# Optimization experiments

Measured on AMD Instinct MI355X. Metric: run time of the kernel, lower is better.

The kernel has to match this reference:

```python
import jax, jax.numpy as jnp
import numpy as np

B, T, M, VM = 64, 512, 8, 50  # batch, time, num_modules, rois per module
EPS = 1e-5  # BatchNorm eps


def setup_inputs() -> dict:
    key = jax.random.key(0)
    ks = jax.random.split(key, 12)
    x = jax.random.normal(ks[0], (B, M * VM, T, 1), jnp.float32)
    # learned adjacency, torch init = ones/V; perturb slightly
    PA = jnp.full((M, VM, VM), 1.0 / VM, jnp.float32) + 0.01 * jax.random.normal(ks[1], (M, VM, VM), jnp.float32)
    conv_w = jax.random.normal(ks[2], (M,), jnp.float32)          # 1x1 conv weight (1->1 chan) per module
    conv_b = 0.1 * jax.random.normal(ks[3], (M,), jnp.float32)
    bn_gamma = 1.0 + 0.1 * jax.random.normal(ks[4], (M,), jnp.float32)
    bn_beta = 0.1 * jax.random.normal(ks[5], (M,), jnp.float32)
    bn_mean = 0.1 * jax.random.normal(ks[6], (M,), jnp.float32)
    bn_var = jax.random.uniform(ks[7], (M,), jnp.float32) + 0.5   # positive
    w1 = jax.random.normal(ks[8], (M, 8), jnp.float32) * 0.5      # Linear(1,8) weight per module
    b1 = 0.1 * jax.random.normal(ks[9], (M, 8), jnp.float32)
    w2 = jax.random.normal(ks[10], (M, 8), jnp.float32) * 0.5     # Linear(8,1) weight per module
    b2 = 0.1 * jax.random.normal(ks[11], (M,), jnp.float32)
    return dict(x=x, PA=PA, conv_w=conv_w, conv_b=conv_b, bn_gamma=bn_gamma, bn_beta=bn_beta,
                bn_mean=bn_mean, bn_var=bn_var, w1=w1, b1=b1, w2=w2, b2=b2)


def reference(x, PA, conv_w, conv_b, bn_gamma, bn_beta, bn_mean, bn_var, w1, b1, w2, b2):
    # x: [B, V_total, T, 1]; torch permute(0,3,2,1) -> [B, C=1, T, V_total]
    xp = x[..., 0].transpose(0, 2, 1)                 # [B, T, V_total]
    xm = xp.reshape(B, T, M, VM)                      # contiguous module blocks == index_select
    # UnitGCN: x_agg = x @ A per module
    agg = jnp.einsum('btmv,mvw->btmw', xm, PA)        # [B, T, M, VM]
    # 1x1 conv (scalar per module) + BatchNorm2d(1) in eval mode + ReLU
    y = agg * conv_w[:, None] + conv_b[:, None]
    scale = bn_gamma / jnp.sqrt(bn_var + EPS)
    h = jax.nn.relu((y - bn_mean[:, None]) * scale[:, None] + bn_beta[:, None])
    # AttentionPooling: MLP(1->8->1) on channel dim, softmax over nodes, weighted sum
    hid = jnp.tanh(h[..., None] * w1[:, None, :] + b1[:, None, :])   # [B, T, M, VM, 8]
    score = jnp.einsum('btmvh,mh->btmv', hid, w2) + b2[:, None]      # [B, T, M, VM]
    attn = jax.nn.softmax(score, axis=3)
    pooled = jnp.sum(h * attn, axis=3)                # [B, T, M]
    # concat over modules on dim 1 -> [B, M, T, 1]
    return pooled.transpose(0, 2, 1)[..., None]
```

## Files before the change

kernel.cpp:

```cpp
#include <hip/hip_runtime.h>

#define BB 64
#define TT 512
#define MM 8
#define VMM 50
#define KP 64
#define NP 64
#define RSTRIDE 36
#define EPSV 1e-5f

#define TN   1024
#define HMAX 16.0f
#define HSTEP (HMAX / TN)
#define INVH  (TN / HMAX)

using short8  = __attribute__((ext_vector_type(8))) short;
using float4v = __attribute__((ext_vector_type(4))) float;

__device__ __forceinline__ float fast_rcp(float x) {
    return __builtin_amdgcn_rcpf(x);
}
__device__ __forceinline__ float fast_tanh(float x) {
    float e2 = __expf(2.0f * x);
    return fmaf(-2.0f, fast_rcp(e2 + 1.0f), 1.0f);
}
__device__ __forceinline__ unsigned f2bf(float f) {
    unsigned u = __float_as_uint(f);
    return (u + 0x7FFFu + ((u >> 16) & 1u)) >> 16;
}
__device__ __forceinline__ unsigned pack2(float lo, float hi) {
    return f2bf(lo) | (f2bf(hi) << 16);
}

__global__ __launch_bounds__(256, 2)
void intra_module_agg_kernel(const float* __restrict__ x,
                             const float* __restrict__ PA,
                             const float* __restrict__ conv_w,
                             const float* __restrict__ conv_b,
                             const float* __restrict__ bn_gamma,
                             const float* __restrict__ bn_beta,
                             const float* __restrict__ bn_mean,
                             const float* __restrict__ bn_var,
                             const float* __restrict__ w1,
                             const float* __restrict__ b1,
                             const float* __restrict__ w2,
                             const float* __restrict__ b2,
                             float* __restrict__ out)
{
    const int blk = blockIdx.x;
    const int tt  = blk & 1;
    const int m   = (blk >> 1) & 7;
    const int b   = blk >> 4;
    const int j   = threadIdx.x;

    __shared__ __align__(16) unsigned xsu[256 * RSTRIDE];
    __shared__ __align__(16) unsigned psu[NP * RSTRIDE];
    __shared__ float  graw[TN + 1];
    __shared__ float2 gtab[TN];

    const float scale = bn_gamma[m] * __frsqrt_rn(bn_var[m] + EPSV);
    const float Amul  = conv_w[m] * scale;
    const float Cadd  = (conv_b[m] - bn_mean[m]) * scale + bn_beta[m];

    {
        const float* xb = x + ((b * (MM * VMM) + m * VMM) * TT + tt * 256 + j);
#pragma unroll
        for (int vp = 0; vp < 25; ++vp) {
            float a = xb[(2 * vp) * TT];
            float c = xb[(2 * vp + 1) * TT];
            xsu[j * RSTRIDE + vp] = pack2(a, c);
        }
#pragma unroll
        for (int vp = 25; vp < 32; ++vp) xsu[j * RSTRIDE + vp] = 0u;
    }

    {
        const float* pa = PA + m * (VMM * VMM);
        const int w  = j & 63;
        const int vb = (j >> 6) * 8;
#pragma unroll
        for (int i = 0; i < 8; ++i) {
            int vp = vb + i, v0 = 2 * vp, v1 = v0 + 1;
            float a = (w < VMM && v0 < VMM) ? pa[v0 * VMM + w] : 0.0f;
            float c = (w < VMM && v1 < VMM) ? pa[v1 * VMM + w] : 0.0f;
            psu[w * RSTRIDE + vp] = pack2(a, c);
        }
    }

    {
        const float B2 = b2[m];
        for (int i = j; i < TN + 1; i += 256) {
            float h = i * HSTEP;
            float s = B2;
#pragma unroll
            for (int k = 0; k < 8; ++k)
                s = fmaf(w2[m * 8 + k],
                         fast_tanh(fmaf(h, w1[m * 8 + k], b1[m * 8 + k])), s);
            graw[i] = __expf(s);
        }
    }
    __syncthreads();

    for (int i = j; i < TN; i += 256)
        gtab[i] = make_float2(graw[i], graw[i + 1] - graw[i]);

    const int lane = j & 63, wv = j >> 6;
    const int q = lane >> 4, nl = lane & 15;

    short8 Bf[4][2];
#pragma unroll
    for (int nt = 0; nt < 4; ++nt)
#pragma unroll
        for (int ks = 0; ks < 2; ++ks)
            Bf[nt][ks] = *(const short8*)&psu[(nt * 16 + nl) * RSTRIDE + ks * 16 + q * 4];

    float4v C[4][4];
#pragma unroll
    for (int mt = 0; mt < 4; ++mt)
#pragma unroll
        for (int nt = 0; nt < 4; ++nt)
            C[mt][nt] = (float4v){0.f, 0.f, 0.f, 0.f};

#pragma unroll
    for (int mt = 0; mt < 4; ++mt) {
        const int row = (wv * 4 + mt) * 16 + nl;
        short8 A0 = *(const short8*)&xsu[row * RSTRIDE + 0 * 16 + q * 4];
        short8 A1 = *(const short8*)&xsu[row * RSTRIDE + 1 * 16 + q * 4];
#pragma unroll
        for (int nt = 0; nt < 4; ++nt) {
            C[mt][nt] = __builtin_amdgcn_mfma_f32_16x16x32_bf16(A0, Bf[nt][0], C[mt][nt], 0, 0, 0);
            C[mt][nt] = __builtin_amdgcn_mfma_f32_16x16x32_bf16(A1, Bf[nt][1], C[mt][nt], 0, 0, 0);
        }
    }
    __syncthreads();

    const int obase = (b * MM + m) * TT + tt * 256;
#pragma unroll
    for (int mt = 0; mt < 4; ++mt) {
        float se[4] = {0.f, 0.f, 0.f, 0.f};
        float sh[4] = {0.f, 0.f, 0.f, 0.f};
#pragma unroll
        for (int nt = 0; nt < 4; ++nt) {
            const bool ok = (nt * 16 + nl) < VMM;
#pragma unroll
            for (int r = 0; r < 4; ++r) {
                float h = fmaxf(fmaf(C[mt][nt][r], Amul, Cadd), 0.0f);
                float u = fminf(h, HMAX - 0.0005f) * INVH;
                int   i = (int)u;
                float fr = u - (float)i;
                float2 p = gtab[i];
                float e = ok ? fmaf(fr, p.y, p.x) : 0.0f;
                se[r] += e;
                sh[r] = fmaf(h, e, sh[r]);
            }
        }
#pragma unroll
        for (int r = 0; r < 4; ++r) {
#pragma unroll
            for (int mk = 1; mk < 16; mk <<= 1) {
                se[r] += __shfl_xor(se[r], mk, 64);
                sh[r] += __shfl_xor(sh[r], mk, 64);
            }
        }
        if (nl == 0) {
#pragma unroll
            for (int r = 0; r < 4; ++r)
                out[obase + (wv * 4 + mt) * 16 + q * 4 + r] = sh[r] * fast_rcp(se[r]);
        }
    }
}

extern "C" void kernel_launch(void* const* d_in, const int* in_sizes, int n_in,
                              void* d_out, int out_size, void* d_ws, size_t ws_size,
                              hipStream_t stream) {
    const float* x        = (const float*)d_in[0];
    const float* PA       = (const float*)d_in[1];
    const float* conv_w   = (const float*)d_in[2];
    const float* conv_b   = (const float*)d_in[3];
    const float* bn_gamma = (const float*)d_in[4];
    const float* bn_beta  = (const float*)d_in[5];
    const float* bn_mean  = (const float*)d_in[6];
    const float* bn_var   = (const float*)d_in[7];
    const float* w1       = (const float*)d_in[8];
    const float* b1       = (const float*)d_in[9];
    const float* w2       = (const float*)d_in[10];
    const float* b2       = (const float*)d_in[11];
    float* out = (float*)d_out;

    dim3 grid(BB * MM * (TT / 256));
    dim3 block(256);
    intra_module_agg_kernel<<<grid, block, 0, stream>>>(
        x, PA, conv_w, conv_b, bn_gamma, bn_beta, bn_mean, bn_var,
        w1, b1, w2, b2, out);
}
```

Before: 116.3 us.

## Halve time tile, transpose MFMA roles, pack fp16 softmax table

Each block now covers 128 time steps instead of 256, so the grid doubles and launch bounds allow 4 blocks per CU. The MFMA operands are swapped so PA is the A operand and x is B. Each lane then holds one time step across many nodes, which cuts the softmax reduction from 4-step shuffles to 2. The exp-score lookup table is built in a single pass into fp16-packed pairs, with a shifted exponent for range, which drops one shared buffer and one barrier. The risks are fp16 precision loss in the table and possible bank conflicts in the new LDS access pattern.

```diff
diff --git a/kernel.cpp b/kernel.cpp
--- a/kernel.cpp
+++ b/kernel.cpp
@@ -4,8 +4,7 @@
 #define TT 512
 #define MM 8
 #define VMM 50
-#define KP 64
-#define NP 64
+#define TBLK 128
 #define RSTRIDE 36
 #define EPSV 1e-5f
 
@@ -31,8 +30,19 @@
 __device__ __forceinline__ unsigned pack2(float lo, float hi) {
     return f2bf(lo) | (f2bf(hi) << 16);
 }
-
-__global__ __launch_bounds__(256, 2)
+__device__ __forceinline__ unsigned packh2(float lo, float hi) {
+    unsigned short a = __builtin_bit_cast(unsigned short, (_Float16)lo);
+    unsigned short b = __builtin_bit_cast(unsigned short, (_Float16)hi);
+    return (unsigned)a | ((unsigned)b << 16);
+}
+__device__ __forceinline__ float h2f_lo(unsigned p) {
+    return (float)__builtin_bit_cast(_Float16, (unsigned short)(p & 0xFFFFu));
+}
+__device__ __forceinline__ float h2f_hi(unsigned p) {
+    return (float)__builtin_bit_cast(_Float16, (unsigned short)(p >> 16));
+}
+
+__global__ __launch_bounds__(256, 4)
 void intra_module_agg_kernel(const float* __restrict__ x,
                              const float* __restrict__ PA,
                              const float* __restrict__ conv_w,
@@ -48,30 +58,36 @@
                              float* __restrict__ out)
 {
     const int blk = blockIdx.x;
-    const int tt  = blk & 1;
-    const int m   = (blk >> 1) & 7;
-    const int b   = blk >> 4;
+    const int tq  = blk & 3;
+    const int m   = (blk >> 2) & 7;
+    const int b   = blk >> 5;
     const int j   = threadIdx.x;
 
-    __shared__ __align__(16) unsigned xsu[256 * RSTRIDE];
-    __shared__ __align__(16) unsigned psu[NP * RSTRIDE];
-    __shared__ float  graw[TN + 1];
-    __shared__ float2 gtab[TN];
+    __shared__ __align__(16) unsigned xsu[TBLK * RSTRIDE];
+    __shared__ __align__(16) unsigned psu[64 * RSTRIDE];
+    __shared__ unsigned gt[TN];
 
     const float scale = bn_gamma[m] * __frsqrt_rn(bn_var[m] + EPSV);
     const float Amul  = conv_w[m] * scale;
     const float Cadd  = (conv_b[m] - bn_mean[m]) * scale + bn_beta[m];
 
     {
-        const float* xb = x + ((b * (MM * VMM) + m * VMM) * TT + tt * 256 + j);
-#pragma unroll
-        for (int vp = 0; vp < 25; ++vp) {
-            float a = xb[(2 * vp) * TT];
-            float c = xb[(2 * vp + 1) * TT];
-            xsu[j * RSTRIDE + vp] = pack2(a, c);
-        }
-#pragma unroll
-        for (int vp = 25; vp < 32; ++vp) xsu[j * RSTRIDE + vp] = 0u;
+        const int t  = j >> 1;
+        const int hf = j & 1;
+        const float* xb = x + ((b * (MM * VMM) + m * VMM) * TT + tq * TBLK + t);
+        unsigned* row = &xsu[t * RSTRIDE];
+        const int vp0 = hf * 13;
+#pragma unroll
+        for (int i = 0; i < 13; ++i) {
+            int vp = vp0 + i;
+            float a = 0.0f, c = 0.0f;
+            if (vp < 25) { a = xb[(2 * vp) * TT]; c = xb[(2 * vp + 1) * TT]; }
+            row[vp] = pack2(a, c);
+        }
+        if (hf) {
+#pragma unroll
+            for (int vp = 26; vp < 32; ++vp) row[vp] = 0u;
+        }
     }
 
     {
@@ -88,85 +104,87 @@
     }
 
     {
-        const float B2 = b2[m];
-        for (int i = j; i < TN + 1; i += 256) {
-            float h = i * HSTEP;
-            float s = B2;
-#pragma unroll
-            for (int k = 0; k < 8; ++k)
-                s = fmaf(w2[m * 8 + k],
-                         fast_tanh(fmaf(h, w1[m * 8 + k], b1[m * 8 + k])), s);
-            graw[i] = __expf(s);
-        }
-    }
+        float W1[8], B1[8], W2[8];
+        float B2 = b2[m], sabs = 0.0f;
+#pragma unroll
+        for (int k = 0; k < 8; ++k) {
+            W1[k] = w1[m * 8 + k];
+            B1[k] = b1[m * 8 + k];
+            W2[k] = w2[m * 8 + k];
+            sabs += fabsf(W2[k]);
+        }
+        const float s0 = (B2 + sabs) - 8.0f;
+        float gv[5];
+#pragma unroll
+        for (int k = 0; k < 5; ++k) {
+            float h = (4 * j + k) * HSTEP;
+            float s = B2 - s0;
+#pragma unroll
+            for (int i = 0; i < 8; ++i)
+                s = fmaf(W2[i], fast_tanh(fmaf(h, W1[i], B1[i])), s);
+            gv[k] = __expf(s);
+        }
+#pragma unroll
+        for (int k = 0; k < 4; ++k)
+            gt[4 * j + k] = packh2(gv[k], gv[k + 1] - gv[k]);
+    }
+
     __syncthreads();
-
-    for (int i = j; i < TN; i += 256)
-        gtab[i] = make_float2(graw[i], graw[i + 1] - graw[i]);
 
     const int lane = j & 63, wv = j >> 6;
     const int q = lane >> 4, nl = lane & 15;
 
-    short8 Bf[4][2];
-#pragma unroll
-    for (int nt = 0; nt < 4; ++nt)
+    short8 A[4][2];
+#pragma unroll
+    for (int wt = 0; wt < 4; ++wt)
 #pragma unroll
         for (int ks = 0; ks < 2; ++ks)
-            Bf[nt][ks] = *(const short8*)&psu[(nt * 16 + nl) * RSTRIDE + ks * 16 + q * 4];
-
-    float4v C[4][4];
-#pragma unroll
-    for (int mt = 0; mt < 4; ++mt)
-#pragma unroll
-        for (int nt = 0; nt < 4; ++nt)
-            C[mt][nt] = (float4v){0.f, 0.f, 0.f, 0.f};
-
-#pragma unroll
-    for (int mt = 0; mt < 4; ++mt) {
-        const int row = (wv * 4 + mt) * 16 + nl;
-        short8 A0 = *(const short8*)&xsu[row * RSTRIDE + 0 * 16 + q * 4];
-        short8 A1 = *(const short8*)&xsu[row * RSTRIDE + 1 * 16 + q * 4];
-#pragma unroll
-        for (int nt = 0; nt < 4; ++nt) {
-            C[mt][nt] = __builtin_amdgcn_mfma_f32_16x16x32_bf16(A0, Bf[nt][0], C[mt][nt], 0, 0, 0);
-            C[mt][nt] = __builtin_amdgcn_mfma_f32_16x16x32_bf16(A1, Bf[nt][1], C[mt][nt], 0, 0, 0);
-        }
-    }
-    __syncthreads();
-
-    const int obase = (b * MM + m) * TT + tt * 256;
-#pragma unroll
-    for (int mt = 0; mt < 4; ++mt) {
-        float se[4] = {0.f, 0.f, 0.f, 0.f};
-        float sh[4] = {0.f, 0.f, 0.f, 0.f};
-#pragma unroll
-        for (int nt = 0; nt < 4; ++nt) {
-            const bool ok = (nt * 16 + nl) < VMM;
+            A[wt][ks] = *(const short8*)&psu[(wt * 16 + nl) * RSTRIDE + ks * 16 + q * 4];
+
+    float4v C[2][4];
+#pragma unroll
+    for (int t2 = 0; t2 < 2; ++t2)
+#pragma unroll
+        for (int wt = 0; wt < 4; ++wt)
+            C[t2][wt] = (float4v){0.f, 0.f, 0.f, 0.f};
+
+#pragma unroll
+    for (int t2 = 0; t2 < 2; ++t2) {
+        const int trow = (wv * 2 + t2) * 16 + nl;
+        short8 Bv0 = *(const short8*)&xsu[trow * RSTRIDE + 0 * 16 + q * 4];
+        short8 Bv1 = *(const short8*)&xsu[trow * RSTRIDE + 1 * 16 + q * 4];
+#pragma unroll
+        for (int wt = 0; wt < 4; ++wt) {
+            C[t2][wt] = __builtin_amdgcn_mfma_f32_16x16x32_bf16(A[wt][0], Bv0, C[t2][wt], 0, 0, 0);
+            C[t2][wt] = __builtin_amdgcn_mfma_f32_16x16x32_bf16(A[wt][1], Bv1, C[t2][wt], 0, 0, 0);
+        }
+    }
+
+    const int obase = (b * MM + m) * TT + tq * TBLK;
+#pragma unroll
+    for (int t2 = 0; t2 < 2; ++t2) {
+        float se = 0.0f, sh = 0.0f;
+#pragma unroll
+        for (int wt = 0; wt < 4; ++wt) {
 #pragma unroll
             for (int r = 0; r < 4; ++r) {
-                float h = fmaxf(fmaf(C[mt][nt][r], Amul, Cadd), 0.0f);
+                const int w = wt * 16 + q * 4 + r;
+                float h = fmaxf(fmaf(C[t2][wt][r], Amul, Cadd), 0.0f);
                 float u = fminf(h, HMAX - 0.0005f) * INVH;
                 int   i = (int)u;
                 float fr = u - (float)i;
-                float2 p = gtab[i];
-                float e = ok ? fmaf(fr, p.y, p.x) : 0.0f;
-                se[r] += e;
-                sh[r] = fmaf(h, e, sh[r]);
+                unsigned p = gt[i];
+                float e = (w < VMM) ? fmaf(fr, h2f_hi(p), h2f_lo(p)) : 0.0f;
+                se += e;
+                sh = fmaf(h, e, sh);
             }
         }
-#pragma unroll
-        for (int r = 0; r < 4; ++r) {
-#pragma unroll
-            for (int mk = 1; mk < 16; mk <<= 1) {
-                se[r] += __shfl_xor(se[r], mk, 64);
-                sh[r] += __shfl_xor(sh[r], mk, 64);
-            }
-        }
-        if (nl == 0) {
-#pragma unroll
-            for (int r = 0; r < 4; ++r)
-                out[obase + (wv * 4 + mt) * 16 + q * 4 + r] = sh[r] * fast_rcp(se[r]);
-        }
+        se += __shfl_xor(se, 16, 64);
+        se += __shfl_xor(se, 32, 64);
+        sh += __shfl_xor(sh, 16, 64);
+        sh += __shfl_xor(sh, 32, 64);
+        if (q == 0)
+            out[obase + (wv * 2 + t2) * 16 + nl] = sh * fast_rcp(se);
     }
 }
 
@@ -187,7 +205,7 @@
     const float* b2       = (const float*)d_in[11];
     float* out = (float*)d_out;
 
-    dim3 grid(BB * MM * (TT / 256));
+    dim3 grid(BB * MM * (TT / TBLK));
     dim3 block(256);
     intra_module_agg_kernel<<<grid, block, 0, stream>>>(
         x, PA, conv_w, conv_b, bn_gamma, bn_beta, bn_mean, bn_var,
```

Result: faster. 113.6 us (-2.3%).
